# Kernel optimization log

Measured on AMD Instinct MI355X. Metric: run time of the kernel, lower is better.

The kernel has to match this reference:

```python
import jax, jax.numpy as jnp
import numpy as np

N = 100000          # num nodes
E = 1600000         # num edges
D = 128             # input_dim == output_dim
H = 8               # heads
C = D // H          # per-head out channels (16)
NEG_SLOPE = 0.2     # PyG GATConv leaky_relu default
LN_EPS = 1e-5


def setup_inputs() -> dict:
    key = jax.random.key(0)
    ks = jax.random.split(key, 8)
    x = jax.random.normal(ks[0], (N, D), dtype=jnp.float32)
    edge_index = jax.random.randint(ks[1], (2, E), 0, N, dtype=jnp.int64)
    scale = 1.0 / np.sqrt(D)
    W = jax.random.normal(ks[2], (D, H * C), dtype=jnp.float32) * scale
    att_src = jax.random.normal(ks[3], (H, C), dtype=jnp.float32) * scale
    att_dst = jax.random.normal(ks[4], (H, C), dtype=jnp.float32) * scale
    bias = jnp.zeros((H * C,), dtype=jnp.float32)
    gamma = jnp.ones((D,), dtype=jnp.float32)
    beta = jnp.zeros((D,), dtype=jnp.float32)
    return {"x": x, "edge_index": edge_index, "W": W, "att_src": att_src,
            "att_dst": att_dst, "bias": bias, "gamma": gamma, "beta": beta}


def reference(x, edge_index, W, att_src, att_dst, bias, gamma, beta):
    src, dst = edge_index[0], edge_index[1]
    # linear transform -> [N, H, C]
    h = (x @ W).reshape(N, H, C)
    # per-node attention terms [N, H]
    a_src = jnp.einsum("nhc,hc->nh", h, att_src)
    a_dst = jnp.einsum("nhc,hc->nh", h, att_dst)
    # per-edge raw scores [E, H]
    e = a_src[src] + a_dst[dst]
    e = jnp.where(e >= 0, e, NEG_SLOPE * e)
    # segment softmax over destination neighborhoods
    m = jax.ops.segment_max(e, dst, num_segments=N)          # [N, H]
    e = jnp.exp(e - m[dst])
    s = jax.ops.segment_sum(e, dst, num_segments=N)          # [N, H]
    alpha = e / (s[dst] + 1e-16)                             # [E, H]
    # weighted scatter-aggregate of source features
    msg = h[src] * alpha[:, :, None]                         # [E, H, C]
    out = jax.ops.segment_sum(msg, dst, num_segments=N).reshape(N, H * C)
    out = out + bias
    # residual (input_dim == output_dim -> identity)
    out = out + x
    # LayerNorm
    mu = jnp.mean(out, axis=-1, keepdims=True)
    var = jnp.var(out, axis=-1, keepdims=True)
    out = (out - mu) * jax.lax.rsqrt(var + LN_EPS) * gamma + beta
    # ReLU (dropout is identity in eval)
    return jax.nn.relu(out)
```

## Files before the change

kernel.cpp:

```cpp
#include <hip/hip_runtime.h>
#include <hip/hip_fp16.h>

#define N_NODES 100000
#define N_EDGES 1600000
#define NEG_SLOPE 0.2f
#define LN_EPS 1e-5f
#define NB 782
#define GEMM_BLOCKS 782
#define BIN_BLOCKS 196
#define BIN_EDGES 8192
#define BUCKET_CAP 4096
#define CSR_CAP 2816

typedef _Float16 f16x8 __attribute__((ext_vector_type(8)));
typedef float f32x4 __attribute__((ext_vector_type(4)));

#define XLDS_LD 136

__global__ __launch_bounds__(256) void gemm_bin_kernel(const float* __restrict__ x,
                                                       const float* __restrict__ W,
                                                       const float* __restrict__ att_src,
                                                       const float* __restrict__ att_dst,
                                                       const int* __restrict__ ei,
                                                       __half* __restrict__ h16,
                                                       __half* __restrict__ a_srcp,
                                                       float* __restrict__ a_dstp,
                                                       int* __restrict__ bucket_cursor,
                                                       unsigned* __restrict__ binned) {
    __shared__ __align__(16) char lds[34816 + 32768];
    const int t = threadIdx.x;

    if (blockIdx.x >= GEMM_BLOCKS) {
        int* hist = reinterpret_cast<int*>(lds);
        int* cbase = reinterpret_cast<int*>(lds + 4096);
        for (int i = t; i < NB; i += 256) hist[i] = 0;
        __syncthreads();
        const int e0 = (blockIdx.x - GEMM_BLOCKS) * BIN_EDGES;
        const int4* dsts = reinterpret_cast<const int4*>(ei + N_EDGES);
        const int b4 = e0 >> 2;
        for (int i = t; i < BIN_EDGES / 4; i += 256) {
            int idx = b4 + i;
            if (idx < N_EDGES / 4) {
                int4 d = dsts[idx];
                atomicAdd(&hist[d.x >> 7], 1);
                atomicAdd(&hist[d.y >> 7], 1);
                atomicAdd(&hist[d.z >> 7], 1);
                atomicAdd(&hist[d.w >> 7], 1);
            }
        }
        __syncthreads();
        for (int i = t; i < NB; i += 256) {
            int c = hist[i];
            cbase[i] = c ? atomicAdd(&bucket_cursor[i], c) : 0;
        }
        __syncthreads();
        for (int i = t; i < NB; i += 256) hist[i] = 0;
        __syncthreads();
        for (int i = t; i < BIN_EDGES; i += 256) {
            int e = e0 + i;
            if (e < N_EDGES) {
                int s_ = ei[e];
                int d = ei[N_EDGES + e];
                int bk = d >> 7;
                int off = atomicAdd(&hist[bk], 1);
                binned[bk * BUCKET_CAP + cbase[bk] + off] = (unsigned)((s_ << 7) | (d & 127));
            }
        }
        return;
    }

    _Float16* x_lds = reinterpret_cast<_Float16*>(lds);
    _Float16* w_frag = reinterpret_cast<_Float16*>(lds + 34816);
    const int nbase = blockIdx.x * 128;
    const int w = t >> 6;
    const int l = t & 63;
    const int lr = l & 15;
    const int lg = l >> 4;

    for (int i = t; i < 2048; i += 256) {
        int r = i >> 4, seg = i & 15;
        int gr = nbase + r;
        gr = gr < N_NODES ? gr : N_NODES - 1;
        const float4 v0 = *reinterpret_cast<const float4*>(&x[(size_t)gr * 128 + seg * 8]);
        const float4 v1 = *reinterpret_cast<const float4*>(&x[(size_t)gr * 128 + seg * 8 + 4]);
        _Float16 hb[8] = {(_Float16)v0.x, (_Float16)v0.y, (_Float16)v0.z, (_Float16)v0.w,
                          (_Float16)v1.x, (_Float16)v1.y, (_Float16)v1.z, (_Float16)v1.w};
        *reinterpret_cast<uint4*>(&x_lds[r * XLDS_LD + seg * 8]) =
            *reinterpret_cast<const uint4*>(hb);
    }
    for (int s = t; s < 2048; s += 256) {
        int ks = s >> 9, ct = (s >> 6) & 7, ln = s & 63;
        int kb = ks * 32 + (ln >> 4) * 8;
        int col = ct * 16 + (ln & 15);
        _Float16 wb[8];
#pragma unroll
        for (int j = 0; j < 8; ++j) wb[j] = (_Float16)W[(size_t)(kb + j) * 128 + col];
        *reinterpret_cast<uint4*>(&w_frag[s * 8]) = *reinterpret_cast<const uint4*>(wb);
    }
    __syncthreads();

    f32x4 acc[2][8] = {};
    const int m0 = w * 32;
#pragma unroll
    for (int ks = 0; ks < 4; ++ks) {
        f16x8 a[2], b[8];
#pragma unroll
        for (int rt = 0; rt < 2; ++rt)
            a[rt] = *reinterpret_cast<const f16x8*>(
                &x_lds[(m0 + rt * 16 + lr) * XLDS_LD + ks * 32 + lg * 8]);
#pragma unroll
        for (int ct = 0; ct < 8; ++ct)
            b[ct] = *reinterpret_cast<const f16x8*>(&w_frag[((ks * 8 + ct) * 64 + l) * 8]);
#pragma unroll
        for (int rt = 0; rt < 2; ++rt)
#pragma unroll
            for (int ct = 0; ct < 8; ++ct)
                acc[rt][ct] = __builtin_amdgcn_mfma_f32_16x16x32_f16(a[rt], b[ct],
                                                                     acc[rt][ct], 0, 0, 0);
    }
    __syncthreads();
#pragma unroll
    for (int rt = 0; rt < 2; ++rt)
#pragma unroll
        for (int ct = 0; ct < 8; ++ct)
#pragma unroll
            for (int reg = 0; reg < 4; ++reg)
                x_lds[(m0 + rt * 16 + lg * 4 + reg) * XLDS_LD + ct * 16 + lr] =
                    (_Float16)acc[rt][ct][reg];
    __syncthreads();
    for (int i = t; i < 2048; i += 256) {
        int r = i >> 4, seg = i & 15;
        int gr = nbase + r;
        if (gr < N_NODES)
            *reinterpret_cast<uint4*>(&h16[(size_t)gr * 128 + seg * 8]) =
                *reinterpret_cast<const uint4*>(&x_lds[r * XLDS_LD + seg * 8]);
    }
    for (int idx = t; idx < 1024; idx += 256) {
        int row = idx >> 3, hd = idx & 7;
        int gr = nbase + row;
        if (gr < N_NODES) {
            float ps = 0.f, pd = 0.f;
#pragma unroll
            for (int j = 0; j < 16; ++j) {
                const float hv = (float)x_lds[row * XLDS_LD + hd * 16 + j];
                ps = fmaf(hv, att_src[hd * 16 + j], ps);
                pd = fmaf(hv, att_dst[hd * 16 + j], pd);
            }
            a_srcp[gr * 8 + hd] = __float2half_rn(ps);
            a_dstp[gr * 8 + hd] = pd;
        }
    }
}

__global__ __launch_bounds__(256) void csr_build_kernel(const unsigned* __restrict__ binned,
                                                        const int* __restrict__ bucket_cursor,
                                                        int* __restrict__ row_beg,
                                                        int* __restrict__ row_end,
                                                        int* __restrict__ csr_src) {
    __shared__ int deg[128];
    __shared__ int sc[128];
    __shared__ int cur[128];
    __shared__ unsigned stage[CSR_CAP];
    const int b = blockIdx.x;
    const int t = threadIdx.x;
    const int pbase = b * BUCKET_CAP;
    const int cnt = bucket_cursor[b];
    const int n0 = b << 7;
    const bool fits = cnt <= CSR_CAP;
    if (t < 128) deg[t] = 0;
    __syncthreads();
    if (fits) {
        for (int i = t; i < cnt; i += 256) {
            unsigned p = binned[pbase + i];
            stage[i] = p;
            atomicAdd(&deg[p & 127], 1);
        }
    } else {
        for (int i = t; i < cnt; i += 256)
            atomicAdd(&deg[binned[pbase + i] & 127], 1);
    }
    __syncthreads();
    if (t < 128) sc[t] = deg[t];
    __syncthreads();
    for (int off = 1; off < 128; off <<= 1) {
        int u = (t < 128 && t >= off) ? sc[t - off] : 0;
        __syncthreads();
        if (t < 128) sc[t] += u;
        __syncthreads();
    }
    if (t < 128) {
        int excl = sc[t] - deg[t];
        cur[t] = excl;
        int n = n0 + t;
        if (n < N_NODES) {
            row_beg[n] = pbase + excl;
            row_end[n] = pbase + excl + deg[t];
        }
    }
    __syncthreads();
    if (fits) {
        for (int i = t; i < cnt; i += 256) {
            unsigned p = stage[i];
            int off = atomicAdd(&cur[p & 127], 1);
            csr_src[pbase + off] = (int)(p >> 7);
        }
    } else {
        for (int i = t; i < cnt; i += 256) {
            unsigned p = binned[pbase + i];
            int off = atomicAdd(&cur[p & 127], 1);
            csr_src[pbase + off] = (int)(p >> 7);
        }
    }
}

__global__ __launch_bounds__(256) void node_aggregate_kernel(const int* __restrict__ row_beg,
                                                             const int* __restrict__ row_end,
                                                             const int* __restrict__ csr_src,
                                                             const __half* __restrict__ h16,
                                                             const __half* __restrict__ a_srcp,
                                                             const float* __restrict__ a_dstp,
                                                             const float* __restrict__ x,
                                                             const float* __restrict__ bias,
                                                             const float* __restrict__ gamma,
                                                             const float* __restrict__ beta,
                                                             float* __restrict__ out) {
    int node = blockIdx.x * 4 + (threadIdx.x >> 6);
    if (node >= N_NODES) return;
    const int lane = threadIdx.x & 63;
    const int q = lane >> 4;
    const int ql = lane & 15;
    const int ch = ql * 8;
    const int head = ql >> 1;

    const float adst = a_dstp[node * 8 + head];

    const int beg = row_beg[node];
    const int end = row_end[node];

    float s = 0.f;
    float accv[8] = {};

    const char* __restrict__ hbase = reinterpret_cast<const char*>(h16);
    const unsigned chb = (unsigned)(ql * 16);

#define LOADH(dst_, sidx_) \
    dst_ = *reinterpret_cast<const uint4*>(hbase + ((unsigned)(sidx_) * 256u + chb))
#define LOADA(dst_, sidx_) dst_ = __half2float(a_srcp[(sidx_) * 8 + head])

#define CONSUME(hv_, av_)                                                  \
    {                                                                      \
        float e = (av_) + adst;                                            \
        e = fmaxf(e, NEG_SLOPE * e);                                       \
        e = fminf(e, 80.f);                                                \
        const float p = __expf(e);                                         \
        s += p;                                                            \
        const __half* hh = reinterpret_cast<const __half*>(&(hv_));        \
        _Pragma("unroll")                                                  \
        for (int j = 0; j < 8; ++j)                                        \
            accv[j] = fmaf(p, __half2float(hh[j]), accv[j]);               \
    }

    int i = beg + q;
    if (i < end) {
        do {
            const bool v1 = (i + 4) < end;
            const bool v2 = (i + 8) < end;
            const bool v3 = (i + 12) < end;
            uint4 h0, h1, h2, h3;
            float a0, a1, a2, a3;
            const int s0 = csr_src[i];
            LOADH(h0, s0); LOADA(a0, s0);
            if (v1) { const int s1 = csr_src[i + 4];  LOADH(h1, s1); LOADA(a1, s1); }
            if (v2) { const int s2 = csr_src[i + 8];  LOADH(h2, s2); LOADA(a2, s2); }
            if (v3) { const int s3 = csr_src[i + 12]; LOADH(h3, s3); LOADA(a3, s3); }
            CONSUME(h0, a0);
            if (v1) CONSUME(h1, a1);
            if (v2) CONSUME(h2, a2);
            if (v3) CONSUME(h3, a3);
            i += 16;
        } while (i < end);
    }
#undef LOADH
#undef LOADA
#undef CONSUME

    s += __shfl_xor(s, 16);
    s += __shfl_xor(s, 32);
#pragma unroll
    for (int j = 0; j < 8; ++j) {
        accv[j] += __shfl_xor(accv[j], 16);
        accv[j] += __shfl_xor(accv[j], 32);
    }

    const float rs = 1.0f / (s + 1e-16f);
    const float* xrp = x + (size_t)node * 128 + ch;
    float v[8];
#pragma unroll
    for (int j = 0; j < 8; ++j) {
        const float xr = __builtin_nontemporal_load(xrp + j);
        v[j] = accv[j] * rs + bias[ch + j] + xr;
    }

    float sum = 0.f, sq = 0.f;
#pragma unroll
    for (int j = 0; j < 8; ++j) {
        sum += v[j];
        sq = fmaf(v[j], v[j], sq);
    }
#pragma unroll
    for (int off = 8; off > 0; off >>= 1) {
        sum += __shfl_xor(sum, off);
        sq += __shfl_xor(sq, off);
    }
    const float mu = sum * (1.0f / 128.0f);
    const float var = sq * (1.0f / 128.0f) - mu * mu;
    const float inv = rsqrtf(var + LN_EPS);
    if (q == 0) {
        float o[8];
#pragma unroll
        for (int j = 0; j < 8; ++j) {
            float tt = (v[j] - mu) * inv * gamma[ch + j] + beta[ch + j];
            o[j] = tt > 0.f ? tt : 0.f;
        }
        float* op = out + (size_t)node * 128 + ch;
#pragma unroll
        for (int j = 0; j < 8; ++j) __builtin_nontemporal_store(o[j], op + j);
    }
}

extern "C" void kernel_launch(void* const* d_in, const int* in_sizes, int n_in,
                              void* d_out, int out_size, void* d_ws, size_t ws_size,
                              hipStream_t stream) {
    const float* x = (const float*)d_in[0];
    const int* ei = (const int*)d_in[1];
    const float* W = (const float*)d_in[2];
    const float* att_src = (const float*)d_in[3];
    const float* att_dst = (const float*)d_in[4];
    const float* bias = (const float*)d_in[5];
    const float* gamma = (const float*)d_in[6];
    const float* beta = (const float*)d_in[7];
    float* out = (float*)d_out;

    char* base = (char*)d_ws;
    __half* h16    = (__half*)base;
    __half* a_srcp = (__half*)(base + 25600000);
    float* a_dstp  = (float*)(base + 27200000);
    int* csr_src   = (int*)(base + 30400000);
    int* row_beg   = (int*)(base + 43212288);
    int* row_end   = (int*)(base + 43612288);
    unsigned* binned = (unsigned*)(base + 44012288);
    int* bucket_cursor = (int*)(base + 56824576);

    hipMemsetAsync(bucket_cursor, 0, NB * sizeof(int), stream);
    gemm_bin_kernel<<<GEMM_BLOCKS + BIN_BLOCKS, 256, 0, stream>>>(
        x, W, att_src, att_dst, ei, h16, a_srcp, a_dstp, bucket_cursor, binned);
    csr_build_kernel<<<NB, 256, 0, stream>>>(binned, bucket_cursor, row_beg, row_end, csr_src);
    node_aggregate_kernel<<<(N_NODES + 3) / 4, 256, 0, stream>>>(
        row_beg, row_end, csr_src, h16, a_srcp, a_dstp, x, bias, gamma, beta, out);
}
```

Baseline: 150.0 us.

## Fuse CSR build into aggregation kernel with per-block LDS CSR

Merges the CSR build and node aggregation kernels into one. Each block reads one destination bucket, keeps the half-bucket's CSR in shared memory and aggregates 64 nodes (16 per wave), so global csr_src/row_beg/row_end traffic and one launch disappear. The inner loop is now a software-pipelined one-edge-per-quarter-wave prefetch instead of a 4-way unrolled batch. Each bucket's binned list is read twice (once per half-block), the larger shared memory footprint may lower occupancy, and lcsr has a fixed 2048 capacity with no overflow fallback, so a very skewed input could overflow it.

```diff
diff --git a/kernel.cpp b/kernel.cpp
--- a/kernel.cpp
+++ b/kernel.cpp
@@ -10,7 +10,6 @@
 #define BIN_BLOCKS 196
 #define BIN_EDGES 8192
 #define BUCKET_CAP 4096
-#define CSR_CAP 2816
 
 typedef _Float16 f16x8 __attribute__((ext_vector_type(8)));
 typedef float f32x4 __attribute__((ext_vector_type(4)));
@@ -152,94 +151,61 @@
     }
 }
 
-__global__ __launch_bounds__(256) void csr_build_kernel(const unsigned* __restrict__ binned,
+__global__ __launch_bounds__(256) void agg_fused_kernel(const unsigned* __restrict__ binned,
                                                         const int* __restrict__ bucket_cursor,
-                                                        int* __restrict__ row_beg,
-                                                        int* __restrict__ row_end,
-                                                        int* __restrict__ csr_src) {
-    __shared__ int deg[128];
-    __shared__ int sc[128];
-    __shared__ int cur[128];
-    __shared__ unsigned stage[CSR_CAP];
-    const int b = blockIdx.x;
+                                                        const __half* __restrict__ h16,
+                                                        const __half* __restrict__ a_srcp,
+                                                        const float* __restrict__ a_dstp,
+                                                        const float* __restrict__ x,
+                                                        const float* __restrict__ bias,
+                                                        const float* __restrict__ gamma,
+                                                        const float* __restrict__ beta,
+                                                        float* __restrict__ out) {
+    __shared__ unsigned stage[BUCKET_CAP];
+    __shared__ int deg[64], sc[64], cur[64];
+    __shared__ int lcsr[2048];
+    const int b = blockIdx.x >> 1;
+    const int half = blockIdx.x & 1;
     const int t = threadIdx.x;
     const int pbase = b * BUCKET_CAP;
     const int cnt = bucket_cursor[b];
-    const int n0 = b << 7;
-    const bool fits = cnt <= CSR_CAP;
-    if (t < 128) deg[t] = 0;
-    __syncthreads();
-    if (fits) {
-        for (int i = t; i < cnt; i += 256) {
-            unsigned p = binned[pbase + i];
-            stage[i] = p;
-            atomicAdd(&deg[p & 127], 1);
-        }
-    } else {
-        for (int i = t; i < cnt; i += 256)
-            atomicAdd(&deg[binned[pbase + i] & 127], 1);
-    }
-    __syncthreads();
-    if (t < 128) sc[t] = deg[t];
-    __syncthreads();
-    for (int off = 1; off < 128; off <<= 1) {
-        int u = (t < 128 && t >= off) ? sc[t - off] : 0;
-        __syncthreads();
-        if (t < 128) sc[t] += u;
-        __syncthreads();
-    }
-    if (t < 128) {
-        int excl = sc[t] - deg[t];
-        cur[t] = excl;
-        int n = n0 + t;
-        if (n < N_NODES) {
-            row_beg[n] = pbase + excl;
-            row_end[n] = pbase + excl + deg[t];
-        }
-    }
-    __syncthreads();
-    if (fits) {
-        for (int i = t; i < cnt; i += 256) {
-            unsigned p = stage[i];
-            int off = atomicAdd(&cur[p & 127], 1);
-            csr_src[pbase + off] = (int)(p >> 7);
-        }
-    } else {
-        for (int i = t; i < cnt; i += 256) {
-            unsigned p = binned[pbase + i];
-            int off = atomicAdd(&cur[p & 127], 1);
-            csr_src[pbase + off] = (int)(p >> 7);
-        }
-    }
-}
-
-__global__ __launch_bounds__(256) void node_aggregate_kernel(const int* __restrict__ row_beg,
-                                                             const int* __restrict__ row_end,
-                                                             const int* __restrict__ csr_src,
-                                                             const __half* __restrict__ h16,
-                                                             const __half* __restrict__ a_srcp,
-                                                             const float* __restrict__ a_dstp,
-                                                             const float* __restrict__ x,
-                                                             const float* __restrict__ bias,
-                                                             const float* __restrict__ gamma,
-                                                             const float* __restrict__ beta,
-                                                             float* __restrict__ out) {
-    int node = blockIdx.x * 4 + (threadIdx.x >> 6);
-    if (node >= N_NODES) return;
-    const int lane = threadIdx.x & 63;
+    const int node0 = (b << 7) + half * 64;
+
+    if (t < 64) deg[t] = 0;
+    __syncthreads();
+    for (int i = t; i < cnt; i += 256) {
+        unsigned p = binned[pbase + i];
+        stage[i] = p;
+        int dl = p & 127;
+        if ((dl >> 6) == half) atomicAdd(&deg[dl & 63], 1);
+    }
+    __syncthreads();
+    if (t < 64) sc[t] = deg[t];
+    __syncthreads();
+    for (int off = 1; off < 64; off <<= 1) {
+        int u = (t < 64 && t >= off) ? sc[t - off] : 0;
+        __syncthreads();
+        if (t < 64) sc[t] += u;
+        __syncthreads();
+    }
+    if (t < 64) cur[t] = sc[t] - deg[t];
+    __syncthreads();
+    for (int i = t; i < cnt; i += 256) {
+        unsigned p = stage[i];
+        int dl = p & 127;
+        if ((dl >> 6) == half) {
+            int off = atomicAdd(&cur[dl & 63], 1);
+            lcsr[off] = (int)(p >> 7);
+        }
+    }
+    __syncthreads();
+
+    const int wave = t >> 6;
+    const int lane = t & 63;
     const int q = lane >> 4;
     const int ql = lane & 15;
     const int ch = ql * 8;
     const int head = ql >> 1;
-
-    const float adst = a_dstp[node * 8 + head];
-
-    const int beg = row_beg[node];
-    const int end = row_end[node];
-
-    float s = 0.f;
-    float accv[8] = {};
-
     const char* __restrict__ hbase = reinterpret_cast<const char*>(h16);
     const unsigned chb = (unsigned)(ql * 16);
 
@@ -247,85 +213,95 @@
     dst_ = *reinterpret_cast<const uint4*>(hbase + ((unsigned)(sidx_) * 256u + chb))
 #define LOADA(dst_, sidx_) dst_ = __half2float(a_srcp[(sidx_) * 8 + head])
 
-#define CONSUME(hv_, av_)                                                  \
-    {                                                                      \
-        float e = (av_) + adst;                                            \
-        e = fmaxf(e, NEG_SLOPE * e);                                       \
-        e = fminf(e, 80.f);                                                \
-        const float p = __expf(e);                                         \
-        s += p;                                                            \
-        const __half* hh = reinterpret_cast<const __half*>(&(hv_));        \
-        _Pragma("unroll")                                                  \
-        for (int j = 0; j < 8; ++j)                                        \
-            accv[j] = fmaf(p, __half2float(hh[j]), accv[j]);               \
-    }
-
-    int i = beg + q;
-    if (i < end) {
-        do {
-            const bool v1 = (i + 4) < end;
-            const bool v2 = (i + 8) < end;
-            const bool v3 = (i + 12) < end;
-            uint4 h0, h1, h2, h3;
-            float a0, a1, a2, a3;
-            const int s0 = csr_src[i];
-            LOADH(h0, s0); LOADA(a0, s0);
-            if (v1) { const int s1 = csr_src[i + 4];  LOADH(h1, s1); LOADA(a1, s1); }
-            if (v2) { const int s2 = csr_src[i + 8];  LOADH(h2, s2); LOADA(a2, s2); }
-            if (v3) { const int s3 = csr_src[i + 12]; LOADH(h3, s3); LOADA(a3, s3); }
-            CONSUME(h0, a0);
-            if (v1) CONSUME(h1, a1);
-            if (v2) CONSUME(h2, a2);
-            if (v3) CONSUME(h3, a3);
-            i += 16;
-        } while (i < end);
+    for (int r = 0; r < 16; ++r) {
+        const int nl = wave * 16 + r;
+        const int node = node0 + nl;
+        if (node >= N_NODES) continue;
+
+        const float adst = a_dstp[node * 8 + head];
+        const int beg = sc[nl] - deg[nl];
+        const int end = sc[nl];
+
+        float s = 0.f;
+        float accv[8] = {};
+
+        int i = beg + q;
+        if (i < end) {
+            const int sF = lcsr[i];
+            int s1 = (i + 4 < end) ? lcsr[i + 4] : sF;
+            uint4 hv;
+            float as;
+            LOADH(hv, sF);
+            LOADA(as, sF);
+            while (true) {
+                const uint4 hc = hv;
+                const float ac = as;
+                const int sN = s1;
+                const int i8 = i + 8;
+                s1 = (i8 < end) ? lcsr[i8] : sF;
+                LOADH(hv, sN);
+                LOADA(as, sN);
+
+                float e = ac + adst;
+                e = fmaxf(e, NEG_SLOPE * e);
+                e = fminf(e, 80.f);
+                const float p = __expf(e);
+                s += p;
+                const __half* hh = reinterpret_cast<const __half*>(&hc);
+#pragma unroll
+                for (int j = 0; j < 8; ++j)
+                    accv[j] = fmaf(p, __half2float(hh[j]), accv[j]);
+
+                i += 4;
+                if (i >= end) break;
+            }
+        }
+
+        s += __shfl_xor(s, 16);
+        s += __shfl_xor(s, 32);
+#pragma unroll
+        for (int j = 0; j < 8; ++j) {
+            accv[j] += __shfl_xor(accv[j], 16);
+            accv[j] += __shfl_xor(accv[j], 32);
+        }
+
+        const float rs = 1.0f / (s + 1e-16f);
+        const float* xrp = x + (size_t)node * 128 + ch;
+        float v[8];
+#pragma unroll
+        for (int j = 0; j < 8; ++j) {
+            const float xr = __builtin_nontemporal_load(xrp + j);
+            v[j] = accv[j] * rs + bias[ch + j] + xr;
+        }
+
+        float sum = 0.f, sq = 0.f;
+#pragma unroll
+        for (int j = 0; j < 8; ++j) {
+            sum += v[j];
+            sq = fmaf(v[j], v[j], sq);
+        }
+#pragma unroll
+        for (int off = 8; off > 0; off >>= 1) {
+            sum += __shfl_xor(sum, off);
+            sq += __shfl_xor(sq, off);
+        }
+        const float mu = sum * (1.0f / 128.0f);
+        const float var = sq * (1.0f / 128.0f) - mu * mu;
+        const float inv = rsqrtf(var + LN_EPS);
+        if (q == 0) {
+            float o[8];
+#pragma unroll
+            for (int j = 0; j < 8; ++j) {
+                float tt = (v[j] - mu) * inv * gamma[ch + j] + beta[ch + j];
+                o[j] = tt > 0.f ? tt : 0.f;
+            }
+            float* op = out + (size_t)node * 128 + ch;
+#pragma unroll
+            for (int j = 0; j < 8; ++j) __builtin_nontemporal_store(o[j], op + j);
+        }
     }
 #undef LOADH
 #undef LOADA
-#undef CONSUME
-
-    s += __shfl_xor(s, 16);
-    s += __shfl_xor(s, 32);
-#pragma unroll
-    for (int j = 0; j < 8; ++j) {
-        accv[j] += __shfl_xor(accv[j], 16);
-        accv[j] += __shfl_xor(accv[j], 32);
-    }
-
-    const float rs = 1.0f / (s + 1e-16f);
-    const float* xrp = x + (size_t)node * 128 + ch;
-    float v[8];
-#pragma unroll
-    for (int j = 0; j < 8; ++j) {
-        const float xr = __builtin_nontemporal_load(xrp + j);
-        v[j] = accv[j] * rs + bias[ch + j] + xr;
-    }
-
-    float sum = 0.f, sq = 0.f;
-#pragma unroll
-    for (int j = 0; j < 8; ++j) {
-        sum += v[j];
-        sq = fmaf(v[j], v[j], sq);
-    }
-#pragma unroll
-    for (int off = 8; off > 0; off >>= 1) {
-        sum += __shfl_xor(sum, off);
-        sq += __shfl_xor(sq, off);
-    }
-    const float mu = sum * (1.0f / 128.0f);
-    const float var = sq * (1.0f / 128.0f) - mu * mu;
-    const float inv = rsqrtf(var + LN_EPS);
-    if (q == 0) {
-        float o[8];
-#pragma unroll
-        for (int j = 0; j < 8; ++j) {
-            float tt = (v[j] - mu) * inv * gamma[ch + j] + beta[ch + j];
-            o[j] = tt > 0.f ? tt : 0.f;
-        }
-        float* op = out + (size_t)node * 128 + ch;
-#pragma unroll
-        for (int j = 0; j < 8; ++j) __builtin_nontemporal_store(o[j], op + j);
-    }
 }
 
 extern "C" void kernel_launch(void* const* d_in, const int* in_sizes, int n_in,
@@ -345,16 +321,12 @@
     __half* h16    = (__half*)base;
     __half* a_srcp = (__half*)(base + 25600000);
     float* a_dstp  = (float*)(base + 27200000);
-    int* csr_src   = (int*)(base + 30400000);
-    int* row_beg   = (int*)(base + 43212288);
-    int* row_end   = (int*)(base + 43612288);
-    unsigned* binned = (unsigned*)(base + 44012288);
-    int* bucket_cursor = (int*)(base + 56824576);
+    unsigned* binned = (unsigned*)(base + 30400000);
+    int* bucket_cursor = (int*)(base + 43212288);
 
     hipMemsetAsync(bucket_cursor, 0, NB * sizeof(int), stream);
     gemm_bin_kernel<<<GEMM_BLOCKS + BIN_BLOCKS, 256, 0, stream>>>(
         x, W, att_src, att_dst, ei, h16, a_srcp, a_dstp, bucket_cursor, binned);
-    csr_build_kernel<<<NB, 256, 0, stream>>>(binned, bucket_cursor, row_beg, row_end, csr_src);
-    node_aggregate_kernel<<<(N_NODES + 3) / 4, 256, 0, stream>>>(
-        row_beg, row_end, csr_src, h16, a_srcp, a_dstp, x, bias, gamma, beta, out);
+    agg_fused_kernel<<<NB * 2, 256, 0, stream>>>(
+        binned, bucket_cursor, h16, a_srcp, a_dstp, x, bias, gamma, beta, out);
 }
```

New measurement: 174.4 us. +16.3%, slower.
